# Optimization experiments

Hardware: AMD Instinct MI355X
Metric: run time of the kernel (lower is better)

Reference implementation:

```python
import jax, jax.numpy as jnp
import numpy as np

N_NODES = 50000


def setup_inputs() -> dict:
    key = jax.random.key(0)
    k1, k2, k3, k4, k5 = jax.random.split(key, 5)
    d_in, d_out, n_edges = 128, 128, 800000
    x = jax.random.normal(k1, (N_NODES, d_in), dtype=jnp.float32)
    edge_index = jax.random.randint(k2, (2, n_edges), 0, N_NODES, dtype=jnp.int64)
    # Glorot-ish init for linear weights, bias zeros-like small normal
    W_l = jax.random.normal(k3, (d_in, d_out), dtype=jnp.float32) / np.sqrt(d_in)
    W_r = jax.random.normal(k4, (d_in, d_out), dtype=jnp.float32) / np.sqrt(d_in)
    b = jax.random.normal(k5, (d_out,), dtype=jnp.float32) * 0.01
    return {"x": x, "edge_index": edge_index, "W_l": W_l, "W_r": W_r, "b": b}


def reference(x, edge_index, W_l, W_r, b):
    # PyG SAGEConv (aggr='mean', root_weight=True, bias=True):
    #   out_i = W_l @ mean_{j: (j->i) in E} x_j + b + W_r @ x_i
    # followed by ReLU (GConv act) and dropout(p=0.0, eval) == identity.
    src, dst = edge_index[0], edge_index[1]
    msgs = x[src]                                            # [E, d_in] gather
    agg_sum = jax.ops.segment_sum(msgs, dst, num_segments=N_NODES)  # [N, d_in]
    deg = jax.ops.segment_sum(jnp.ones_like(dst, dtype=x.dtype), dst,
                              num_segments=N_NODES)          # [N]
    agg_mean = agg_sum / jnp.maximum(deg, 1.0)[:, None]      # zero for isolated nodes
    z = agg_mean @ W_l + b + x @ W_r                         # [N, d_out]
    return jax.nn.relu(z)
```

## Files before the change

### kernel.cpp

```cpp
#include <hip/hip_runtime.h>

#define N_NODES 50000
#define D 128
#define SCAN_NBLK 49

typedef short bf16x8 __attribute__((ext_vector_type(8)));
typedef float f32x4 __attribute__((ext_vector_type(4)));
typedef float f32x2 __attribute__((ext_vector_type(2)));

__device__ __forceinline__ ushort f2bf(float f) {
    uint u = __float_as_uint(f);
    u += 0x7FFF + ((u >> 16) & 1);
    return (ushort)(u >> 16);
}

__device__ __forceinline__ void addrow_fp8(int4 q, float* a) {
    f32x2 p;
    p = __builtin_amdgcn_cvt_pk_f32_fp8(q.x, false); a[0]  += p.x; a[1]  += p.y;
    p = __builtin_amdgcn_cvt_pk_f32_fp8(q.x, true);  a[2]  += p.x; a[3]  += p.y;
    p = __builtin_amdgcn_cvt_pk_f32_fp8(q.y, false); a[4]  += p.x; a[5]  += p.y;
    p = __builtin_amdgcn_cvt_pk_f32_fp8(q.y, true);  a[6]  += p.x; a[7]  += p.y;
    p = __builtin_amdgcn_cvt_pk_f32_fp8(q.z, false); a[8]  += p.x; a[9]  += p.y;
    p = __builtin_amdgcn_cvt_pk_f32_fp8(q.z, true);  a[10] += p.x; a[11] += p.y;
    p = __builtin_amdgcn_cvt_pk_f32_fp8(q.w, false); a[12] += p.x; a[13] += p.y;
    p = __builtin_amdgcn_cvt_pk_f32_fp8(q.w, true);  a[14] += p.x; a[15] += p.y;
}

__global__ __launch_bounds__(256) void convert_kernel(const float* __restrict__ x,
                                                      const float* __restrict__ Wl,
                                                      const float* __restrict__ Wr,
                                                      ushort* __restrict__ x_bf,
                                                      int* __restrict__ x_fp8,
                                                      ushort* __restrict__ Btf) {
    const int i = blockIdx.x * 256 + threadIdx.x;
    if (i < (N_NODES * D) / 4) {
        float4 v = ((const float4*)x)[i];
        ushort4 o;
        o.x = f2bf(v.x); o.y = f2bf(v.y); o.z = f2bf(v.z); o.w = f2bf(v.w);
        ((ushort4*)x_bf)[i] = o;
        int p = __builtin_amdgcn_cvt_pk_fp8_f32(v.x, v.y, 0, false);
        p = __builtin_amdgcn_cvt_pk_fp8_f32(v.z, v.w, p, true);
        x_fp8[i] = p;
    }
    if (i < 32768) {
        int j  = i & 7;
        int l  = (i >> 3) & 63;
        int nf = (i >> 9) & 7;
        int ks = (i >> 12) & 7;
        int lr = l & 15, kb = l >> 4;
        int col  = nf * 16 + lr;
        int kloc = (ks & 3) * 32 + kb * 8 + j;
        const float* W = (ks < 4) ? Wl : Wr;
        Btf[i] = f2bf(W[kloc * D + col]);
    }
}

__global__ void hist_rank_kernel(const int* __restrict__ dst, int* __restrict__ deg,
                                 ushort* __restrict__ rank, int E) {
    int e = blockIdx.x * 256 + threadIdx.x;
    if (e < E) rank[e] = (ushort)atomicAdd(&deg[dst[e]], 1);
}

__global__ __launch_bounds__(256) void scanA_kernel(const int* __restrict__ deg,
                                                    int* __restrict__ offsets,
                                                    int* __restrict__ blocksums) {
    __shared__ int wsums[4];
    __shared__ int wbase[4];
    const int t = threadIdx.x;
    const int lane = t & 63;
    const int wid = t >> 6;
    const int base = blockIdx.x * 1024 + t * 4;

    int v0 = 0, v1 = 0, v2 = 0, v3 = 0;
    if (base + 3 < N_NODES) {
        int4 q = *(const int4*)&deg[base];
        v0 = q.x; v1 = q.y; v2 = q.z; v3 = q.w;
    } else {
        if (base + 0 < N_NODES) v0 = deg[base + 0];
        if (base + 1 < N_NODES) v1 = deg[base + 1];
        if (base + 2 < N_NODES) v2 = deg[base + 2];
        if (base + 3 < N_NODES) v3 = deg[base + 3];
    }
    int tsum = v0 + v1 + v2 + v3;

    int sc = tsum;
    #pragma unroll
    for (int off = 1; off < 64; off <<= 1) {
        int u = __shfl_up(sc, off);
        if (lane >= off) sc += u;
    }
    if (lane == 63) wsums[wid] = sc;
    __syncthreads();
    if (t == 0) {
        int c = 0;
        #pragma unroll
        for (int w = 0; w < 4; ++w) { wbase[w] = c; c += wsums[w]; }
    }
    __syncthreads();

    int excl = wbase[wid] + sc - tsum;
    int o0 = excl, o1 = o0 + v0, o2 = o1 + v1, o3 = o2 + v2;
    if (base + 3 < N_NODES) {
        *(int4*)&offsets[base] = make_int4(o0, o1, o2, o3);
    } else {
        if (base + 0 < N_NODES) offsets[base + 0] = o0;
        if (base + 1 < N_NODES) offsets[base + 1] = o1;
        if (base + 2 < N_NODES) offsets[base + 2] = o2;
        if (base + 3 < N_NODES) offsets[base + 3] = o3;
    }
    if (t == 255) blocksums[blockIdx.x] = excl + tsum;
}

__global__ __launch_bounds__(256) void scanBC_kernel(int* __restrict__ offsets,
                                                     const int* __restrict__ blocksums,
                                                     int E) {
    __shared__ int sbase;
    const int t = threadIdx.x;
    const int b = blockIdx.x;
    if (t < 64) {
        int v = (t < b) ? blocksums[t] : 0;
        #pragma unroll
        for (int off = 32; off > 0; off >>= 1) v += __shfl_down(v, off);
        if (t == 0) sbase = v;
    }
    __syncthreads();
    const int add = sbase;
    int base = b * 1024 + t * 4;
    if (base + 3 < N_NODES) {
        int4 q = *(int4*)&offsets[base];
        q.x += add; q.y += add; q.z += add; q.w += add;
        *(int4*)&offsets[base] = q;
    } else {
        if (base + 0 < N_NODES) offsets[base + 0] += add;
        if (base + 1 < N_NODES) offsets[base + 1] += add;
        if (base + 2 < N_NODES) offsets[base + 2] += add;
    }
    if (b == SCAN_NBLK - 1 && t == 0) offsets[N_NODES] = E;
}

__global__ void scatter_kernel(const int* __restrict__ src, const int* __restrict__ dst,
                               const int* __restrict__ offsets, const ushort* __restrict__ rank,
                               ushort* __restrict__ sorted_src, int E) {
    int e = blockIdx.x * 256 + threadIdx.x;
    if (e < E) {
        int d = dst[e];
        sorted_src[offsets[d] + (int)rank[e]] = (ushort)src[e];
    }
}

__global__ __launch_bounds__(256) void aggregate_fp8(const int* __restrict__ x_fp8,
                                                     const ushort* __restrict__ sorted_src,
                                                     const int* __restrict__ offsets,
                                                     ushort* __restrict__ agg_bf) {
    const int g = threadIdx.x >> 3;
    const int j = threadIdx.x & 7;
    const int node = blockIdx.x * 32 + g;
    if (node >= N_NODES) return;
    const int s = offsets[node];
    const int e = offsets[node + 1];

    float a[16];
    #pragma unroll
    for (int k = 0; k < 16; ++k) a[k] = 0.0f;

    const int4* xq = (const int4*)x_fp8;
    int p = s;
    for (; p + 4 <= e; p += 4) {
        int s0 = sorted_src[p + 0];
        int s1 = sorted_src[p + 1];
        int s2 = sorted_src[p + 2];
        int s3 = sorted_src[p + 3];
        int4 q0 = xq[s0 * 8 + j];
        int4 q1 = xq[s1 * 8 + j];
        int4 q2 = xq[s2 * 8 + j];
        int4 q3 = xq[s3 * 8 + j];
        addrow_fp8(q0, a); addrow_fp8(q1, a); addrow_fp8(q2, a); addrow_fp8(q3, a);
    }
    for (; p < e; ++p) {
        int s0 = sorted_src[p];
        int4 q0 = xq[s0 * 8 + j];
        addrow_fp8(q0, a);
    }
    const int dcnt = e - s;
    const float scale = (dcnt > 0) ? (1.0f / (float)dcnt) : 0.0f;
    ushort tmp[16];
    #pragma unroll
    for (int k = 0; k < 16; ++k) tmp[k] = f2bf(a[k] * scale);
    *(int4*)&agg_bf[node * D + j * 16] = ((int4*)tmp)[0];
    *(int4*)&agg_bf[node * D + j * 16 + 8] = ((int4*)tmp)[1];
}

__global__ __launch_bounds__(256) void gemm_direct(const ushort* __restrict__ agg_bf,
                                                   const ushort* __restrict__ x_bf,
                                                   const ushort* __restrict__ Btf,
                                                   const float* __restrict__ bias,
                                                   float* __restrict__ out) {
    const int t = threadIdx.x;
    const int w = t >> 6;
    const int l = t & 63;
    const int lr = l & 15;
    const int kb = l >> 4;
    const int n0 = blockIdx.x * 64;

    int r = n0 + w * 16 + lr;
    if (r >= N_NODES) r = N_NODES - 1;

    f32x4 acc[8] = {};

    #pragma unroll
    for (int ks = 0; ks < 8; ++ks) {
        bf16x8 af = (ks < 4)
            ? *(const bf16x8*)&agg_bf[r * D + ks * 32 + kb * 8]
            : *(const bf16x8*)&x_bf[r * D + (ks - 4) * 32 + kb * 8];
        const ushort* bp = Btf + (size_t)(ks * 8 * 64 + l) * 8;
        #pragma unroll
        for (int nf = 0; nf < 8; ++nf) {
            bf16x8 bfr = *(const bf16x8*)&bp[nf * 64 * 8];
            acc[nf] = __builtin_amdgcn_mfma_f32_16x16x32_bf16(af, bfr, acc[nf], 0, 0, 0);
        }
    }

    #pragma unroll
    for (int nf = 0; nf < 8; ++nf) {
        const int col = nf * 16 + lr;
        const float bb = bias[col];
        #pragma unroll
        for (int i = 0; i < 4; ++i) {
            int row = n0 + w * 16 + kb * 4 + i;
            if (row < N_NODES)
                out[row * D + col] = fmaxf(acc[nf][i] + bb, 0.0f);
        }
    }
}

extern "C" void kernel_launch(void* const* d_in, const int* in_sizes, int n_in,
                              void* d_out, int out_size, void* d_ws, size_t ws_size,
                              hipStream_t stream) {
    const float* x  = (const float*)d_in[0];
    const int*   ei = (const int*)d_in[1];
    const float* Wl = (const float*)d_in[2];
    const float* Wr = (const float*)d_in[3];
    const float* b  = (const float*)d_in[4];
    float* out = (float*)d_out;

    const int E = in_sizes[1] / 2;
    const int* src = ei;
    const int* dst = ei + E;

    char* wsp = (char*)d_ws;
    int*    deg       = (int*)(wsp + 0);
    int*    offsets   = (int*)(wsp + 200064);
    int*    blocksums = (int*)(wsp + 400192);
    ushort* rank      = (ushort*)(wsp + 400448);
    ushort* sorted    = (ushort*)(wsp + 2000448);
    ushort* x_bf      = (ushort*)(wsp + 3600480);
    ushort* agg_bf    = (ushort*)(wsp + 16400480);
    int*    x_fp8     = (int*)(wsp + 29200480);
    ushort* Btf       = (ushort*)(wsp + 35600480);

    hipMemsetAsync(deg, 0, 50016 * sizeof(int), stream);
    hist_rank_kernel<<<(E + 255) / 256, 256, 0, stream>>>(dst, deg, rank, E);
    convert_kernel<<<(N_NODES * D / 4 + 255) / 256, 256, 0, stream>>>(
        x, Wl, Wr, x_bf, x_fp8, Btf);
    scanA_kernel<<<SCAN_NBLK, 256, 0, stream>>>(deg, offsets, blocksums);
    scanBC_kernel<<<SCAN_NBLK, 256, 0, stream>>>(offsets, blocksums, E);
    scatter_kernel<<<(E + 255) / 256, 256, 0, stream>>>(src, dst, offsets, rank, sorted, E);
    aggregate_fp8<<<(N_NODES + 31) / 32, 256, 0, stream>>>(x_fp8, sorted, offsets, agg_bf);
    gemm_direct<<<(N_NODES + 63) / 64, 256, 0, stream>>>(agg_bf, x_bf, Btf, b, out);
}
```

Baseline: 113.6 us.

## Replace global-atomic CSR build with per-chunk LDS histograms and column scan

Replaces the global atomic histogram/rank pass with 128 chunk blocks that each count destination degrees in a packed 16-bit LDS histogram. A scan over chunks then produces per-chunk base offsets alongside the global prefix sum. The scatter recomputes local ranks with LDS atomics. This removes contended global atomics and the rank array and drops the memset, at the cost of writing and reading 128×50000 partial counts and using only 128 blocks for the count and scatter passes.

```diff
diff --git a/kernel.cpp b/kernel.cpp
--- a/kernel.cpp
+++ b/kernel.cpp
@@ -2,7 +2,8 @@
 
 #define N_NODES 50000
 #define D 128
-#define SCAN_NBLK 49
+#define NC 128
+#define SCANB 196
 
 typedef short bf16x8 __attribute__((ext_vector_type(8)));
 typedef float f32x4 __attribute__((ext_vector_type(4)));
@@ -55,35 +56,46 @@
     }
 }
 
-__global__ void hist_rank_kernel(const int* __restrict__ dst, int* __restrict__ deg,
-                                 ushort* __restrict__ rank, int E) {
-    int e = blockIdx.x * 256 + threadIdx.x;
-    if (e < E) rank[e] = (ushort)atomicAdd(&deg[dst[e]], 1);
-}
-
-__global__ __launch_bounds__(256) void scanA_kernel(const int* __restrict__ deg,
-                                                    int* __restrict__ offsets,
-                                                    int* __restrict__ blocksums) {
+__global__ __launch_bounds__(256) void countA_kernel(const int* __restrict__ dst,
+                                                     ushort* __restrict__ partial,
+                                                     int E, int chunk) {
+    __shared__ uint cnt[N_NODES / 2];
+    const int t = threadIdx.x;
+    const int b = blockIdx.x;
+    for (int k = t; k < N_NODES / 2; k += 256) cnt[k] = 0;
+    __syncthreads();
+    const int e0 = b * chunk;
+    const int e1 = min(E, e0 + chunk);
+    for (int e = e0 + t; e < e1; e += 256) {
+        int d = dst[e];
+        atomicAdd(&cnt[d >> 1], 1u << ((d & 1) << 4));
+    }
+    __syncthreads();
+    uint* pu = (uint*)(partial + (size_t)b * N_NODES);
+    for (int k = t; k < N_NODES / 2; k += 256) pu[k] = cnt[k];
+}
+
+__global__ __launch_bounds__(256) void scanAB_kernel(const ushort* __restrict__ partial,
+                                                     ushort* __restrict__ cumbase,
+                                                     int* __restrict__ offsets,
+                                                     int* __restrict__ blocksums) {
     __shared__ int wsums[4];
     __shared__ int wbase[4];
     const int t = threadIdx.x;
     const int lane = t & 63;
     const int wid = t >> 6;
-    const int base = blockIdx.x * 1024 + t * 4;
-
-    int v0 = 0, v1 = 0, v2 = 0, v3 = 0;
-    if (base + 3 < N_NODES) {
-        int4 q = *(const int4*)&deg[base];
-        v0 = q.x; v1 = q.y; v2 = q.z; v3 = q.w;
-    } else {
-        if (base + 0 < N_NODES) v0 = deg[base + 0];
-        if (base + 1 < N_NODES) v1 = deg[base + 1];
-        if (base + 2 < N_NODES) v2 = deg[base + 2];
-        if (base + 3 < N_NODES) v3 = deg[base + 3];
-    }
-    int tsum = v0 + v1 + v2 + v3;
-
-    int sc = tsum;
+    const int n = blockIdx.x * 256 + t;
+
+    int s = 0;
+    if (n < N_NODES) {
+        #pragma unroll 4
+        for (int c = 0; c < NC; ++c) {
+            int v = (int)partial[(size_t)c * N_NODES + n];
+            cumbase[(size_t)c * N_NODES + n] = (ushort)s;
+            s += v;
+        }
+    }
+    int sc = s;
     #pragma unroll
     for (int off = 1; off < 64; off <<= 1) {
         int u = __shfl_up(sc, off);
@@ -94,57 +106,54 @@
     if (t == 0) {
         int c = 0;
         #pragma unroll
-        for (int w = 0; w < 4; ++w) { wbase[w] = c; c += wsums[w]; }
-    }
-    __syncthreads();
-
-    int excl = wbase[wid] + sc - tsum;
-    int o0 = excl, o1 = o0 + v0, o2 = o1 + v1, o3 = o2 + v2;
-    if (base + 3 < N_NODES) {
-        *(int4*)&offsets[base] = make_int4(o0, o1, o2, o3);
-    } else {
-        if (base + 0 < N_NODES) offsets[base + 0] = o0;
-        if (base + 1 < N_NODES) offsets[base + 1] = o1;
-        if (base + 2 < N_NODES) offsets[base + 2] = o2;
-        if (base + 3 < N_NODES) offsets[base + 3] = o3;
-    }
-    if (t == 255) blocksums[blockIdx.x] = excl + tsum;
-}
-
-__global__ __launch_bounds__(256) void scanBC_kernel(int* __restrict__ offsets,
-                                                     const int* __restrict__ blocksums,
-                                                     int E) {
+        for (int w = 0; w < 4; ++w) { int tmp = wsums[w]; wbase[w] = c; c += tmp; }
+        blocksums[blockIdx.x] = c;
+    }
+    __syncthreads();
+    if (n < N_NODES) offsets[n] = wbase[wid] + sc - s;
+}
+
+__global__ __launch_bounds__(256) void scanBC2_kernel(int* __restrict__ offsets,
+                                                      const int* __restrict__ blocksums,
+                                                      int E) {
+    __shared__ int ws2[4];
     __shared__ int sbase;
     const int t = threadIdx.x;
+    const int lane = t & 63;
+    const int wid = t >> 6;
     const int b = blockIdx.x;
-    if (t < 64) {
-        int v = (t < b) ? blocksums[t] : 0;
-        #pragma unroll
-        for (int off = 32; off > 0; off >>= 1) v += __shfl_down(v, off);
-        if (t == 0) sbase = v;
-    }
-    __syncthreads();
-    const int add = sbase;
-    int base = b * 1024 + t * 4;
-    if (base + 3 < N_NODES) {
-        int4 q = *(int4*)&offsets[base];
-        q.x += add; q.y += add; q.z += add; q.w += add;
-        *(int4*)&offsets[base] = q;
-    } else {
-        if (base + 0 < N_NODES) offsets[base + 0] += add;
-        if (base + 1 < N_NODES) offsets[base + 1] += add;
-        if (base + 2 < N_NODES) offsets[base + 2] += add;
-    }
-    if (b == SCAN_NBLK - 1 && t == 0) offsets[N_NODES] = E;
-}
-
-__global__ void scatter_kernel(const int* __restrict__ src, const int* __restrict__ dst,
-                               const int* __restrict__ offsets, const ushort* __restrict__ rank,
-                               ushort* __restrict__ sorted_src, int E) {
-    int e = blockIdx.x * 256 + threadIdx.x;
-    if (e < E) {
+    int v = (t < b) ? blocksums[t] : 0;
+    #pragma unroll
+    for (int off = 32; off > 0; off >>= 1) v += __shfl_down(v, off);
+    if (lane == 0) ws2[wid] = v;
+    __syncthreads();
+    if (t == 0) sbase = ws2[0] + ws2[1] + ws2[2] + ws2[3];
+    __syncthreads();
+    const int n = b * 256 + t;
+    if (n < N_NODES) offsets[n] += sbase;
+    if (b == SCANB - 1 && t == 0) offsets[N_NODES] = E;
+}
+
+__global__ __launch_bounds__(256) void scatterC_kernel(const int* __restrict__ src,
+                                                       const int* __restrict__ dst,
+                                                       const int* __restrict__ offsets,
+                                                       const ushort* __restrict__ cumbase,
+                                                       ushort* __restrict__ sorted_src,
+                                                       int E, int chunk) {
+    __shared__ uint cnt[N_NODES / 2];
+    const int t = threadIdx.x;
+    const int b = blockIdx.x;
+    for (int k = t; k < N_NODES / 2; k += 256) cnt[k] = 0;
+    __syncthreads();
+    const ushort* cb = cumbase + (size_t)b * N_NODES;
+    const int e0 = b * chunk;
+    const int e1 = min(E, e0 + chunk);
+    for (int e = e0 + t; e < e1; e += 256) {
         int d = dst[e];
-        sorted_src[offsets[d] + (int)rank[e]] = (ushort)src[e];
+        uint prev = atomicAdd(&cnt[d >> 1], 1u << ((d & 1) << 4));
+        int lrank = (int)((prev >> ((d & 1) << 4)) & 0xFFFFu);
+        int pos = offsets[d] + (int)cb[d] + lrank;
+        sorted_src[pos] = (ushort)src[e];
     }
 }
 
@@ -246,25 +255,25 @@
     const int E = in_sizes[1] / 2;
     const int* src = ei;
     const int* dst = ei + E;
+    const int chunk = (E + NC - 1) / NC;
 
     char* wsp = (char*)d_ws;
-    int*    deg       = (int*)(wsp + 0);
-    int*    offsets   = (int*)(wsp + 200064);
-    int*    blocksums = (int*)(wsp + 400192);
-    ushort* rank      = (ushort*)(wsp + 400448);
-    ushort* sorted    = (ushort*)(wsp + 2000448);
-    ushort* x_bf      = (ushort*)(wsp + 3600480);
-    ushort* agg_bf    = (ushort*)(wsp + 16400480);
-    int*    x_fp8     = (int*)(wsp + 29200480);
-    ushort* Btf       = (ushort*)(wsp + 35600480);
-
-    hipMemsetAsync(deg, 0, 50016 * sizeof(int), stream);
-    hist_rank_kernel<<<(E + 255) / 256, 256, 0, stream>>>(dst, deg, rank, E);
+    int*    offsets   = (int*)(wsp + 0);
+    int*    blocksums = (int*)(wsp + 200192);
+    ushort* sorted    = (ushort*)(wsp + 201216);
+    ushort* partial   = (ushort*)(wsp + 1801280);
+    ushort* cumbase   = (ushort*)(wsp + 14601280);
+    ushort* x_bf      = (ushort*)(wsp + 27401280);
+    ushort* agg_bf    = (ushort*)(wsp + 40201280);
+    int*    x_fp8     = (int*)(wsp + 53001280);
+    ushort* Btf       = (ushort*)(wsp + 59401280);
+
     convert_kernel<<<(N_NODES * D / 4 + 255) / 256, 256, 0, stream>>>(
         x, Wl, Wr, x_bf, x_fp8, Btf);
-    scanA_kernel<<<SCAN_NBLK, 256, 0, stream>>>(deg, offsets, blocksums);
-    scanBC_kernel<<<SCAN_NBLK, 256, 0, stream>>>(offsets, blocksums, E);
-    scatter_kernel<<<(E + 255) / 256, 256, 0, stream>>>(src, dst, offsets, rank, sorted, E);
+    countA_kernel<<<NC, 256, 0, stream>>>(dst, partial, E, chunk);
+    scanAB_kernel<<<SCANB, 256, 0, stream>>>(partial, cumbase, offsets, blocksums);
+    scanBC2_kernel<<<SCANB, 256, 0, stream>>>(offsets, blocksums, E);
+    scatterC_kernel<<<NC, 256, 0, stream>>>(src, dst, offsets, cumbase, sorted, E, chunk);
     aggregate_fp8<<<(N_NODES + 31) / 32, 256, 0, stream>>>(x_fp8, sorted, offsets, agg_bf);
     gemm_direct<<<(N_NODES + 63) / 64, 256, 0, stream>>>(agg_bf, x_bf, Btf, b, out);
 }
```

New measurement: 110.6 us. 1.03x faster.
